# Kernel optimization log

Hardware: AMD Instinct MI355X
Metric: run time of the kernel (lower is better)

Reference implementation:

```python
import jax, jax.numpy as jnp
import numpy as np
import math

HEADS = 8
DIM_HEAD = 64
EMB = 512
GROUPS = 32
EPS = 100000.0  # module's literal default norm_eps


def setup_inputs() -> dict:
    key = jax.random.key(0)
    ks = jax.random.split(key, 11)
    B, D, H, W = 2, EMB, 64, 64
    s = 1.0 / math.sqrt(EMB)
    inp = {
        "input": jax.random.normal(ks[0], (B, D, H, W), dtype=jnp.float32),
        "gn_gamma": jnp.ones((EMB,), dtype=jnp.float32),
        "gn_beta": jnp.zeros((EMB,), dtype=jnp.float32),
        "wq": jax.random.normal(ks[1], (EMB, EMB), dtype=jnp.float32) * s,
        "bq": jax.random.normal(ks[2], (EMB,), dtype=jnp.float32) * 0.01,
        "wk": jax.random.normal(ks[3], (EMB, EMB), dtype=jnp.float32) * s,
        "bk": jax.random.normal(ks[4], (EMB,), dtype=jnp.float32) * 0.01,
        "wv": jax.random.normal(ks[5], (EMB, EMB), dtype=jnp.float32) * s,
        "bv": jax.random.normal(ks[6], (EMB,), dtype=jnp.float32) * 0.01,
        "wo": jax.random.normal(ks[7], (EMB, EMB), dtype=jnp.float32) * s,
        "bo": jax.random.normal(ks[8], (EMB,), dtype=jnp.float32) * 0.01,
    }
    return inp


def reference(input, gn_gamma, gn_beta, wq, bq, wk, bk, wv, bv, wo, bo):
    B, D, H, W = input.shape
    S = H * W
    residual = input

    # GroupNorm(32, D) over (C/G, H, W) per group, affine per-channel
    xg = input.reshape(B, GROUPS, (D // GROUPS) * H * W)
    mu = jnp.mean(xg, axis=-1, keepdims=True)
    var = jnp.var(xg, axis=-1, keepdims=True)
    xn = (xg - mu) / jnp.sqrt(var + EPS)
    xn = xn.reshape(B, D, H, W) * gn_gamma[:, None, None] + gn_beta[:, None, None]

    # (B, D, H, W) -> (B, S, D)
    x = xn.reshape(B, D, S).transpose(0, 2, 1)

    # projections (torch Linear: y = x @ W.T + b)
    q = (x @ wq.T + bq).reshape(B, S, HEADS, DIM_HEAD).transpose(0, 2, 1, 3)
    k = (x @ wk.T + bk).reshape(B, S, HEADS, DIM_HEAD).transpose(0, 2, 1, 3)
    v = (x @ wv.T + bv).reshape(B, S, HEADS, DIM_HEAD).transpose(0, 2, 1, 3)

    scale = 1.0 / math.sqrt(DIM_HEAD)
    scores = jnp.einsum("bhqd,bhkd->bhqk", q * scale, k)  # [B, h, S, S]
    attn = jax.nn.softmax(scores, axis=-1)
    o = jnp.einsum("bhqk,bhkd->bhqd", attn, v)  # [B, h, S, dh]
    o = o.transpose(0, 2, 1, 3).reshape(B, S, D)

    out = o @ wo.T + bo  # [B, S, D]
    out = out.transpose(0, 2, 1).reshape(B, D, H, W)
    return out + residual
```

## Files before the change

### kernel.cpp

```cpp
#include <hip/hip_runtime.h>

#define EMB 512
#define SEQ 4096
#define BATCH 2
#define NH 8
#define DH 64
#define GN_EPS 100000.0f
#define ALPHA 0.125f

typedef __bf16 bf16;
typedef __bf16 bf16x8 __attribute__((ext_vector_type(8)));
typedef float f32x4 __attribute__((ext_vector_type(4)));

typedef __attribute__((address_space(1))) unsigned int u32g;
typedef __attribute__((address_space(3))) unsigned int u32l;
__device__ __forceinline__ void gll16(const void* g, void* l) {
  __builtin_amdgcn_global_load_lds((const u32g*)g, (u32l*)l, 16, 0, 0);
}

__device__ __forceinline__ void stage8(const bf16* g, size_t rowStride, bf16* lds, int lane) {
  const int r = lane >> 3, cc = (lane & 7) ^ r;
  gll16(g + (size_t)r * rowStride + cc * 8, lds + lane * 8);
}
__device__ __forceinline__ bf16x8 frag(const bf16* lds, int r, int cc) {
  return *(const bf16x8*)&lds[(((r << 3) + (cc ^ (r & 7))) << 3)];
}

__global__ __launch_bounds__(256) void stats_k(const float* __restrict__ in,
                                               float* __restrict__ rs,
                                               float* __restrict__ ss) {
  const int row = blockIdx.x;
  const float4* p = (const float4*)(in + (size_t)row * SEQ);
  float s = 0.f, s2 = 0.f;
#pragma unroll
  for (int i = 0; i < 4; ++i) {
    float4 v = p[i * 256 + threadIdx.x];
    s += v.x + v.y + v.z + v.w;
    s2 += v.x * v.x + v.y * v.y + v.z * v.z + v.w * v.w;
  }
#pragma unroll
  for (int o = 32; o > 0; o >>= 1) {
    s += __shfl_down(s, o, 64);
    s2 += __shfl_down(s2, o, 64);
  }
  __shared__ float red[8];
  const int wave = threadIdx.x >> 6, lane = threadIdx.x & 63;
  if (lane == 0) { red[wave] = s; red[4 + wave] = s2; }
  __syncthreads();
  if (threadIdx.x == 0) {
    rs[row] = red[0] + red[1] + red[2] + red[3];
    ss[row] = red[4] + red[5] + red[6] + red[7];
  }
}

__global__ __launch_bounds__(256) void prep_k(const float* __restrict__ wq, const float* __restrict__ wk,
                                              const float* __restrict__ wv, const float* __restrict__ wo,
                                              const float* __restrict__ bv,
                                              const float* __restrict__ rs, const float* __restrict__ ss,
                                              const float* __restrict__ gamma, const float* __restrict__ beta,
                                              bf16* __restrict__ wqt, bf16* __restrict__ wkb,
                                              bf16* __restrict__ wvb, bf16* __restrict__ wob,
                                              float* __restrict__ kxa, float* __restrict__ vsuma) {
  __shared__ float t[64][65];
  __shared__ float xs[1024];
  __shared__ float gmu[64], grs[64];
  const int y = blockIdx.y, tid = threadIdx.x;
  if (y < 8) {
    const int c0 = blockIdx.x * 64, r0 = y * 64;
#pragma unroll
    for (int p = 0; p < 16; ++p) {
      int lin = p * 256 + tid;
      int rl = lin >> 6, cl = lin & 63;
      t[rl][cl] = wq[(size_t)(r0 + rl) * EMB + c0 + cl];
    }
    __syncthreads();
#pragma unroll
    for (int p = 0; p < 16; ++p) {
      int lin = p * 256 + tid;
      int cl = lin >> 6, rl = lin & 63;
      wqt[(size_t)(c0 + cl) * EMB + r0 + rl] = (bf16)t[rl][cl];
    }
  } else {
    const int wi = y - 8;
    const float* W = wi == 0 ? wk : wi == 1 ? wv : wo;
    bf16* WO = wi == 0 ? wkb : wi == 1 ? wvb : wob;
    if (wi < 2) {
      if (tid < 64) {
        float s = 0.f, s2 = 0.f;
#pragma unroll
        for (int c = 0; c < 16; ++c) { s += rs[tid * 16 + c]; s2 += ss[tid * 16 + c]; }
        float mu = s * (1.f / 65536.f);
        float var = s2 * (1.f / 65536.f) - mu * mu;
        gmu[tid] = mu;
        grs[tid] = rsqrtf(var + GN_EPS);
      }
      __syncthreads();
      for (int idx = tid; idx < 1024; idx += 256) {
        int d = idx & 511;
        float s = grs[idx >> 4] * gamma[d];
        float tt = beta[d] - gmu[idx >> 4] * s;
        xs[idx] = s * rs[idx] + 4096.f * tt;
      }
      __syncthreads();
    }
    const int n = blockIdx.x * 64 + (tid >> 2);
    const float* Wr = W + (size_t)n * EMB;
    float dot0 = 0.f, dot1 = 0.f;
    const int dq = (tid & 3) * 128;
    for (int d = dq; d < dq + 128; d += 4) {
      float4 w4 = *(const float4*)&Wr[d];
      if (wi < 2) {
        float4 x0 = *(const float4*)&xs[d];
        float4 x1 = *(const float4*)&xs[EMB + d];
        dot0 += w4.x * x0.x + w4.y * x0.y + w4.z * x0.z + w4.w * x0.w;
        dot1 += w4.x * x1.x + w4.y * x1.y + w4.z * x1.z + w4.w * x1.w;
      }
      bf16 r[4] = {(bf16)w4.x, (bf16)w4.y, (bf16)w4.z, (bf16)w4.w};
      *(uint2*)&WO[(size_t)n * EMB + d] = *(uint2*)r;
    }
    if (wi < 2) {
      dot0 += __shfl_xor(dot0, 1, 4); dot0 += __shfl_xor(dot0, 2, 4);
      dot1 += __shfl_xor(dot1, 1, 4); dot1 += __shfl_xor(dot1, 2, 4);
      if ((tid & 3) == 0) {
        if (wi == 0) { kxa[n] = dot0; kxa[EMB + n] = dot1; }
        else { vsuma[n] = dot0 + 4096.f * bv[n]; vsuma[EMB + n] = dot1 + 4096.f * bv[n]; }
      }
    }
  }
}

__global__ __launch_bounds__(256) void nx_k(const float* __restrict__ in,
                                            const float* __restrict__ rs,
                                            const float* __restrict__ ss,
                                            const float* __restrict__ gamma,
                                            const float* __restrict__ beta,
                                            bf16* __restrict__ xds,
                                            bf16* __restrict__ xsd) {
  __shared__ float t[64][65];
  __shared__ float gmu4[4], grs4[4], scl[64], ttl[64];
  const int s0 = blockIdx.x * 64, d0 = blockIdx.y * 64, b = blockIdx.z;
  const int tid = threadIdx.x;
  if (tid < 4) {
    float s = 0.f, s2 = 0.f;
    int base = b * EMB + d0 + tid * 16;
#pragma unroll
    for (int c = 0; c < 16; ++c) { s += rs[base + c]; s2 += ss[base + c]; }
    float mu = s * (1.f / 65536.f);
    float var = s2 * (1.f / 65536.f) - mu * mu;
    gmu4[tid] = mu;
    grs4[tid] = rsqrtf(var + GN_EPS);
  }
  __syncthreads();
  if (tid < 64) {
    int d = d0 + tid;
    float s = grs4[tid >> 4] * gamma[d];
    scl[tid] = s;
    ttl[tid] = beta[d] - gmu4[tid >> 4] * s;
  }
  __syncthreads();
#pragma unroll
  for (int p = 0; p < 16; ++p) {
    int lin = p * 256 + tid;
    int dl = lin >> 6, sl = lin & 63;
    size_t idx = ((size_t)b * EMB + d0 + dl) * SEQ + s0 + sl;
    float v = in[idx] * scl[dl] + ttl[dl];
    t[dl][sl] = v;
    xds[idx] = (bf16)v;
  }
  __syncthreads();
#pragma unroll
  for (int p = 0; p < 16; ++p) {
    int lin = p * 256 + tid;
    int sl = lin >> 6, dl = lin & 63;
    xsd[((size_t)b * SEQ + s0 + sl) * EMB + d0 + dl] = (bf16)t[dl][sl];
  }
}

__global__ __launch_bounds__(256) void graw2_k(const bf16* __restrict__ xds,
                                               float* __restrict__ pG) {
  __shared__ __align__(16) bf16 As[64 * 64];
  __shared__ __align__(16) bf16 Bs[64 * 64];
  int ti = 0, rem = blockIdx.x;
  while (rem >= 8 - ti) { rem -= 8 - ti; ++ti; }
  const int i0 = ti * 64, j0 = (ti + rem) * 64;
  const int kc = blockIdx.y, b = blockIdx.z;
  const bf16* X = xds + (size_t)b * EMB * SEQ;
  const int tid = threadIdx.x;
  const int wave = tid >> 6, lane = tid & 63, l16 = lane & 15, quad = lane >> 4;
  f32x4 acc[4] = {};
  for (int k0 = kc * 512; k0 < kc * 512 + 512; k0 += 64) {
#pragma unroll
    for (int p = 0; p < 2; ++p) {
      int g = wave * 2 + p;
      stage8(&X[(size_t)(i0 + g * 8) * SEQ + k0], SEQ, &As[g * 512], lane);
      stage8(&X[(size_t)(j0 + g * 8) * SEQ + k0], SEQ, &Bs[g * 512], lane);
    }
    __syncthreads();
#pragma unroll
    for (int kt = 0; kt < 2; ++kt) {
      bf16x8 af = frag(As, wave * 16 + l16, kt * 4 + quad);
#pragma unroll
      for (int nt = 0; nt < 4; ++nt) {
        bf16x8 bb = frag(Bs, nt * 16 + l16, kt * 4 + quad);
        acc[nt] = __builtin_amdgcn_mfma_f32_16x16x32_bf16(af, bb, acc[nt], 0, 0, 0);
      }
    }
    __syncthreads();
  }
  float* pg = pG + ((size_t)(b * 8 + kc) * 36 + blockIdx.x) * 4096;
#pragma unroll
  for (int nt = 0; nt < 4; ++nt)
#pragma unroll
    for (int r = 0; r < 4; ++r)
      pg[(wave * 16 + quad * 4 + r) * 64 + nt * 16 + l16] = acc[nt][r];
}

__global__ __launch_bounds__(256) void gsum_k(const float* __restrict__ pG,
                                              bf16* __restrict__ G) {
  const int b = blockIdx.x >> 10;
  const int e = ((blockIdx.x & 1023) << 8) + threadIdx.x;
  const int i = e >> 9, j = e & 511;
  int ti = i >> 6, tj = j >> 6, row = i & 63, col = j & 63;
  if (ti > tj) { int tmp = ti; ti = tj; tj = tmp; tmp = row; row = col; col = tmp; }
  const int tile = ti * 8 - (ti * (ti - 1)) / 2 + (tj - ti);
  const float* p = pG + (size_t)b * 8 * 36 * 4096 + (size_t)tile * 4096 + row * 64 + col;
  float s = 0.f;
#pragma unroll
  for (int kc = 0; kc < 8; ++kc) s += p[(size_t)kc * 36 * 4096];
  G[(size_t)b * 262144 + e] = (bf16)s;
}

__global__ __launch_bounds__(256) void t2pt_k(const bf16* __restrict__ wkb,
                                              const bf16* __restrict__ G,
                                              const bf16* __restrict__ wvb,
                                              float* __restrict__ pPt) {
  __shared__ __align__(16) bf16 As[64 * 64];
  __shared__ __align__(16) bf16 Bs[64 * 64];
  __shared__ __align__(16) bf16 Ps[4 * 16 * 72];
  const int n0 = blockIdx.x * 64, h = blockIdx.y, b = blockIdx.z;
  const int bh = b * NH + h;
  const int tid = threadIdx.x;
  const int wave = tid >> 6, lane = tid & 63, l16 = lane & 15, quad = lane >> 4;
  bf16* Pw = &Ps[wave * 16 * 72];
  f32x4 acc[4] = {};
  for (int k0 = 0; k0 < EMB; k0 += 64) {
#pragma unroll
    for (int p = 0; p < 2; ++p) {
      int g = wave * 2 + p;
      stage8(&wkb[(size_t)(h * DH + g * 8) * EMB + k0], EMB, &As[g * 512], lane);
      stage8(&G[((size_t)b * EMB + n0 + g * 8) * EMB + k0], EMB, &Bs[g * 512], lane);
    }
    __syncthreads();
#pragma unroll
    for (int kt = 0; kt < 2; ++kt) {
      bf16x8 af = frag(As, wave * 16 + l16, kt * 4 + quad);
#pragma unroll
      for (int nt = 0; nt < 4; ++nt) {
        bf16x8 bb = frag(Bs, nt * 16 + l16, kt * 4 + quad);
        acc[nt] = __builtin_amdgcn_mfma_f32_16x16x32_bf16(af, bb, acc[nt], 0, 0, 0);
      }
    }
    __syncthreads();
  }
#pragma unroll
  for (int nt = 0; nt < 4; ++nt)
#pragma unroll
    for (int r = 0; r < 4; ++r)
      Pw[(quad * 4 + r) * 72 + nt * 16 + l16] = (bf16)acc[nt][r];
#pragma unroll
  for (int p = 0; p < 2; ++p) {
    int g = wave * 2 + p;
    stage8(&wvb[(size_t)(h * DH + g * 8) * EMB + n0], EMB, &Bs[g * 512], lane);
  }
  __syncthreads();
  f32x4 accP[4] = {};
#pragma unroll
  for (int kt = 0; kt < 2; ++kt) {
    bf16x8 pf = *(const bf16x8*)&Pw[l16 * 72 + kt * 32 + quad * 8];
#pragma unroll
    for (int nt = 0; nt < 4; ++nt) {
      bf16x8 bb = frag(Bs, nt * 16 + l16, kt * 4 + quad);
      accP[nt] = __builtin_amdgcn_mfma_f32_16x16x32_bf16(pf, bb, accP[nt], 0, 0, 0);
    }
  }
  float* pp = pPt + ((size_t)bh * 8 + blockIdx.x) * 4096;
#pragma unroll
  for (int nt = 0; nt < 4; ++nt)
#pragma unroll
    for (int r = 0; r < 4; ++r)
      pp[(wave * 16 + quad * 4 + r) * 64 + nt * 16 + l16] = accP[nt][r];
}

__global__ __launch_bounds__(256) void ptsum_k(const float* __restrict__ pPt,
                                               const float* __restrict__ bk,
                                               const float* __restrict__ bv,
                                               const float* __restrict__ kxa,
                                               const float* __restrict__ vsuma,
                                               bf16* __restrict__ Pt) {
  const int bh = blockIdx.x;
  const int b = bh >> 3, h = bh & 7;
  const float sfac = ALPHA / 4096.f;
  for (int e = threadIdx.x; e < 4096; e += 256) {
    int kd = e >> 6, vd = e & 63;
    const float* p = pPt + (size_t)bh * 8 * 4096 + e;
    float s = 0.f;
#pragma unroll
    for (int nt = 0; nt < 8; ++nt) s += p[nt * 4096];
    float bvv = bv[h * DH + vd];
    float bkv = bk[h * DH + kd];
    float vx = vsuma[b * EMB + h * DH + vd] - 4096.f * bvv;
    float val = s + kxa[b * EMB + h * DH + kd] * bvv + bkv * vx + 4096.f * bkv * bvv;
    Pt[(size_t)bh * 4096 + e] = (bf16)(val * sfac);
  }
}

__global__ __launch_bounds__(256) void fchain_k(const bf16* __restrict__ wob,
                                                const bf16* __restrict__ Pt,
                                                const bf16* __restrict__ wqt,
                                                const float* __restrict__ wo,
                                                const float* __restrict__ bo,
                                                const float* __restrict__ bq,
                                                const float* __restrict__ vsuma,
                                                bf16* __restrict__ F,
                                                float* __restrict__ cst) {
  __shared__ __align__(16) bf16 Awo[64 * 64];
  __shared__ __align__(16) bf16 Bp[64 * 64];
  __shared__ __align__(16) bf16 Bwq[64 * 64];
  __shared__ __align__(16) bf16 Ps[4 * 16 * 72];
  __shared__ float yc[512];
  const int i0 = blockIdx.x * 64, j0 = blockIdx.y * 64, b = blockIdx.z;
  const int tid = threadIdx.x;
  const int wave = tid >> 6, lane = tid & 63, l16 = lane & 15, quad = lane >> 4;
  bf16* Pw = &Ps[wave * 16 * 72];
  f32x4 accF[4] = {};
  for (int h = 0; h < NH; ++h) {
    __syncthreads();
#pragma unroll
    for (int p = 0; p < 2; ++p) {
      int g = wave * 2 + p;
      stage8(&wob[(size_t)(i0 + g * 8) * EMB + h * DH], EMB, &Awo[g * 512], lane);
      stage8(&Pt[((size_t)(b * NH + h) * DH + g * 8) * DH], DH, &Bp[g * 512], lane);
      stage8(&wqt[(size_t)(j0 + g * 8) * EMB + h * DH], EMB, &Bwq[g * 512], lane);
    }
    __syncthreads();
    f32x4 at[4] = {};
#pragma unroll
    for (int kt = 0; kt < 2; ++kt) {
      bf16x8 af = frag(Awo, wave * 16 + l16, kt * 4 + quad);
#pragma unroll
      for (int nt = 0; nt < 4; ++nt) {
        bf16x8 bb = frag(Bp, nt * 16 + l16, kt * 4 + quad);
        at[nt] = __builtin_amdgcn_mfma_f32_16x16x32_bf16(af, bb, at[nt], 0, 0, 0);
      }
    }
#pragma unroll
    for (int nt = 0; nt < 4; ++nt)
#pragma unroll
      for (int r = 0; r < 4; ++r)
        Pw[(quad * 4 + r) * 72 + nt * 16 + l16] = (bf16)at[nt][r];
#pragma unroll
    for (int kt = 0; kt < 2; ++kt) {
      bf16x8 pf = *(const bf16x8*)&Pw[l16 * 72 + kt * 32 + quad * 8];
#pragma unroll
      for (int nt = 0; nt < 4; ++nt) {
        bf16x8 bb = frag(Bwq, nt * 16 + l16, kt * 4 + quad);
        accF[nt] = __builtin_amdgcn_mfma_f32_16x16x32_bf16(pf, bb, accF[nt], 0, 0, 0);
      }
    }
  }
#pragma unroll
  for (int nt = 0; nt < 4; ++nt)
#pragma unroll
    for (int r = 0; r < 4; ++r)
      F[((size_t)b * EMB + i0 + wave * 16 + quad * 4 + r) * EMB + j0 + nt * 16 + l16] =
          (bf16)accF[nt][r];
  if (j0 == 0) {
    __syncthreads();
    for (int e = tid; e < 512; e += 256) {
      int h = e >> 6, vd = e & 63;
      const bf16* pp = &Pt[(size_t)(b * NH + h) * DH * DH + vd];
      const float* bqh = &bq[h * DH];
      float a = 0.f;
#pragma unroll 8
      for (int kd = 0; kd < 64; ++kd) a += (float)pp[kd * DH] * bqh[kd];
      yc[e] = vsuma[b * EMB + e] * (1.f / 4096.f) + a;
    }
    __syncthreads();
    const int row = i0 + (tid >> 2);
    const float* wr = &wo[(size_t)row * EMB + (tid & 3) * 128];
    const float* yq = &yc[(tid & 3) * 128];
    float a = 0.f;
    for (int e = 0; e < 128; e += 4) {
      float4 w4 = *(const float4*)&wr[e];
      a += w4.x * yq[e] + w4.y * yq[e + 1] + w4.z * yq[e + 2] + w4.w * yq[e + 3];
    }
    a += __shfl_xor(a, 1, 4);
    a += __shfl_xor(a, 2, 4);
    if ((tid & 3) == 0) cst[b * EMB + row] = bo[row] + a;
  }
}

__global__ __launch_bounds__(256) void final_k(const bf16* __restrict__ F,
                                               const bf16* __restrict__ xsd,
                                               const float* __restrict__ cst,
                                               const float* __restrict__ in,
                                               float* __restrict__ out) {
  __shared__ __align__(16) bf16 As[128 * 64];
  __shared__ __align__(16) bf16 Bs[64 * 64];
  const int m0 = blockIdx.x * 128, s0 = blockIdx.y * 64, b = blockIdx.z;
  const bf16* Fb = F + (size_t)b * EMB * EMB;
  const bf16* Xb = xsd + (size_t)b * SEQ * EMB;
  const int tid = threadIdx.x;
  const int wave = tid >> 6, lane = tid & 63, l16 = lane & 15, quad = lane >> 4;
  f32x4 acc[2][4] = {};
  for (int k0 = 0; k0 < EMB; k0 += 64) {
#pragma unroll
    for (int p = 0; p < 4; ++p) {
      int g = wave * 4 + p;
      stage8(&Fb[(size_t)(m0 + g * 8) * EMB + k0], EMB, &As[g * 512], lane);
    }
#pragma unroll
    for (int p = 0; p < 2; ++p) {
      int g = wave * 2 + p;
      stage8(&Xb[(size_t)(s0 + g * 8) * EMB + k0], EMB, &Bs[g * 512], lane);
    }
    __syncthreads();
#pragma unroll
    for (int kt = 0; kt < 2; ++kt) {
      bf16x8 a0 = frag(As, wave * 32 + l16, kt * 4 + quad);
      bf16x8 a1 = frag(As, wave * 32 + 16 + l16, kt * 4 + quad);
#pragma unroll
      for (int nt = 0; nt < 4; ++nt) {
        bf16x8 bb = frag(Bs, nt * 16 + l16, kt * 4 + quad);
        acc[0][nt] = __builtin_amdgcn_mfma_f32_16x16x32_bf16(a0, bb, acc[0][nt], 0, 0, 0);
        acc[1][nt] = __builtin_amdgcn_mfma_f32_16x16x32_bf16(a1, bb, acc[1][nt], 0, 0, 0);
      }
    }
    __syncthreads();
  }
#pragma unroll
  for (int mt = 0; mt < 2; ++mt) {
    int rowl = m0 + wave * 32 + mt * 16 + quad * 4;
#pragma unroll
    for (int r = 0; r < 4; ++r) {
      float cv = cst[b * EMB + rowl + r];
      size_t base = ((size_t)b * EMB + rowl + r) * SEQ + s0;
#pragma unroll
      for (int nt = 0; nt < 4; ++nt) {
        size_t idx = base + nt * 16 + l16;
        out[idx] = in[idx] + cv + acc[mt][nt][r];
      }
    }
  }
}

extern "C" void kernel_launch(void* const* d_in, const int* in_sizes, int n_in,
                              void* d_out, int out_size, void* d_ws, size_t ws_size,
                              hipStream_t stream) {
  const float* inp = (const float*)d_in[0];
  const float* gam = (const float*)d_in[1];
  const float* bet = (const float*)d_in[2];
  const float* wq = (const float*)d_in[3];
  const float* bq = (const float*)d_in[4];
  const float* wk = (const float*)d_in[5];
  const float* bk = (const float*)d_in[6];
  const float* wv = (const float*)d_in[7];
  const float* bv = (const float*)d_in[8];
  const float* wo = (const float*)d_in[9];
  const float* bo = (const float*)d_in[10];
  float* out = (float*)d_out;
  (void)in_sizes; (void)n_in; (void)out_size; (void)ws_size;

  char* ws = (char*)d_ws;
  size_t off = 0;
  auto take = [&](size_t bytes) -> char* {
    char* p = ws + off;
    off += (bytes + 255) & ~(size_t)255;
    return p;
  };
  float* rs = (float*)take(1024 * 4);
  float* ssq = (float*)take(1024 * 4);
  float* kxa = (float*)take(1024 * 4);
  float* vsuma = (float*)take(1024 * 4);
  float* cst = (float*)take(1024 * 4);
  const size_t WB = (size_t)EMB * EMB * sizeof(bf16);
  bf16* wkb = (bf16*)take(WB);
  bf16* wvb = (bf16*)take(WB);
  bf16* wob = (bf16*)take(WB);
  bf16* wqtb = (bf16*)take(WB);
  const size_t XB = (size_t)BATCH * SEQ * EMB * sizeof(bf16);
  bf16* xds = (bf16*)take(XB);
  bf16* xsd = (bf16*)take(XB);
  float* pG = (float*)take((size_t)BATCH * 8 * 36 * 4096 * sizeof(float));
  bf16* G = (bf16*)take((size_t)BATCH * EMB * EMB * sizeof(bf16));
  float* pPt = (float*)take((size_t)16 * 8 * 4096 * sizeof(float));
  bf16* Pt = (bf16*)take((size_t)16 * 4096 * sizeof(bf16));
  bf16* F = (bf16*)take((size_t)BATCH * EMB * EMB * sizeof(bf16));

  stats_k<<<1024, 256, 0, stream>>>(inp, rs, ssq);
  prep_k<<<dim3(8, 11), 256, 0, stream>>>(wq, wk, wv, wo, bv, rs, ssq, gam, bet,
                                          wqtb, wkb, wvb, wob, kxa, vsuma);
  nx_k<<<dim3(64, 8, 2), 256, 0, stream>>>(inp, rs, ssq, gam, bet, xds, xsd);
  graw2_k<<<dim3(36, 8, 2), 256, 0, stream>>>(xds, pG);
  gsum_k<<<2048, 256, 0, stream>>>(pG, G);
  t2pt_k<<<dim3(8, 8, 2), 256, 0, stream>>>(wkb, G, wvb, pPt);
  ptsum_k<<<16, 256, 0, stream>>>(pPt, bk, bv, kxa, vsuma, Pt);
  fchain_k<<<dim3(8, 8, 2), 256, 0, stream>>>(wob, Pt, wqtb, wo, bo, bq, vsuma, F, cst);
  final_k<<<dim3(4, 64, 2), 256, 0, stream>>>(F, xsd, cst, inp, out);
}
```

Measured before the change: 177.3 us.

## Merge prep and normalize kernels, fold split-K reductions into last-block epilogues

Merges the weight-prep and normalize/transpose kernels into one launch. It also removes the separate gsum and ptsum reduction kernels: the last block to finish each tile, found with an atomic counter zeroed in stats_k, does the split-K sum inside graw2_k and t2pt_k. t2pt_k is split over K into twice as many blocks for more parallelism. This cuts the launch count from nine to six and raises occupancy, at the cost of atomics, thread fences and serialized tail reductions in the final blocks.

```diff
diff --git a/kernel.cpp b/kernel.cpp
--- a/kernel.cpp
+++ b/kernel.cpp
@@ -28,7 +28,9 @@
 
 __global__ __launch_bounds__(256) void stats_k(const float* __restrict__ in,
                                                float* __restrict__ rs,
-                                               float* __restrict__ ss) {
+                                               float* __restrict__ ss,
+                                               int* __restrict__ cnt) {
+  if (blockIdx.x == 0 && threadIdx.x < 88) cnt[threadIdx.x] = 0;
   const int row = blockIdx.x;
   const float4* p = (const float4*)(in + (size_t)row * SEQ);
   float s = 0.f, s2 = 0.f;
@@ -53,133 +55,132 @@
   }
 }
 
-__global__ __launch_bounds__(256) void prep_k(const float* __restrict__ wq, const float* __restrict__ wk,
-                                              const float* __restrict__ wv, const float* __restrict__ wo,
-                                              const float* __restrict__ bv,
-                                              const float* __restrict__ rs, const float* __restrict__ ss,
-                                              const float* __restrict__ gamma, const float* __restrict__ beta,
-                                              bf16* __restrict__ wqt, bf16* __restrict__ wkb,
-                                              bf16* __restrict__ wvb, bf16* __restrict__ wob,
-                                              float* __restrict__ kxa, float* __restrict__ vsuma) {
+__global__ __launch_bounds__(256) void nxprep_k(const float* __restrict__ in,
+                                                const float* __restrict__ rs, const float* __restrict__ ss,
+                                                const float* __restrict__ gamma, const float* __restrict__ beta,
+                                                const float* __restrict__ wq, const float* __restrict__ wk,
+                                                const float* __restrict__ wv, const float* __restrict__ wo,
+                                                const float* __restrict__ bv,
+                                                bf16* __restrict__ xds, bf16* __restrict__ xsd,
+                                                bf16* __restrict__ wqt, bf16* __restrict__ wkb,
+                                                bf16* __restrict__ wvb, bf16* __restrict__ wob,
+                                                float* __restrict__ kxa, float* __restrict__ vsuma) {
   __shared__ float t[64][65];
   __shared__ float xs[1024];
   __shared__ float gmu[64], grs[64];
-  const int y = blockIdx.y, tid = threadIdx.x;
-  if (y < 8) {
-    const int c0 = blockIdx.x * 64, r0 = y * 64;
+  const int id = blockIdx.x, tid = threadIdx.x;
+  if (id < 1024) {
+    const int b = id >> 9, rem = id & 511;
+    const int d0 = (rem >> 6) * 64, s0 = (rem & 63) * 64;
+    if (tid < 4) {
+      float s = 0.f, s2 = 0.f;
+      int base = b * EMB + d0 + tid * 16;
+#pragma unroll
+      for (int c = 0; c < 16; ++c) { s += rs[base + c]; s2 += ss[base + c]; }
+      float mu = s * (1.f / 65536.f);
+      float var = s2 * (1.f / 65536.f) - mu * mu;
+      gmu[tid] = mu;
+      grs[tid] = rsqrtf(var + GN_EPS);
+    }
+    __syncthreads();
+    if (tid < 64) {
+      int d = d0 + tid;
+      float s = grs[tid >> 4] * gamma[d];
+      xs[tid] = s;
+      xs[64 + tid] = beta[d] - gmu[tid >> 4] * s;
+    }
+    __syncthreads();
 #pragma unroll
     for (int p = 0; p < 16; ++p) {
       int lin = p * 256 + tid;
-      int rl = lin >> 6, cl = lin & 63;
-      t[rl][cl] = wq[(size_t)(r0 + rl) * EMB + c0 + cl];
+      int dl = lin >> 6, sl = lin & 63;
+      size_t idx = ((size_t)b * EMB + d0 + dl) * SEQ + s0 + sl;
+      float v = in[idx] * xs[dl] + xs[64 + dl];
+      t[dl][sl] = v;
+      xds[idx] = (bf16)v;
     }
     __syncthreads();
 #pragma unroll
     for (int p = 0; p < 16; ++p) {
       int lin = p * 256 + tid;
-      int cl = lin >> 6, rl = lin & 63;
-      wqt[(size_t)(c0 + cl) * EMB + r0 + rl] = (bf16)t[rl][cl];
+      int sl = lin >> 6, dl = lin & 63;
+      xsd[((size_t)b * SEQ + s0 + sl) * EMB + d0 + dl] = (bf16)t[dl][sl];
     }
   } else {
-    const int wi = y - 8;
-    const float* W = wi == 0 ? wk : wi == 1 ? wv : wo;
-    bf16* WO = wi == 0 ? wkb : wi == 1 ? wvb : wob;
-    if (wi < 2) {
-      if (tid < 64) {
-        float s = 0.f, s2 = 0.f;
-#pragma unroll
-        for (int c = 0; c < 16; ++c) { s += rs[tid * 16 + c]; s2 += ss[tid * 16 + c]; }
-        float mu = s * (1.f / 65536.f);
-        float var = s2 * (1.f / 65536.f) - mu * mu;
-        gmu[tid] = mu;
-        grs[tid] = rsqrtf(var + GN_EPS);
+    const int r = id - 1024;
+    const int bx = r & 7, y = r >> 3;
+    if (y < 8) {
+      const int c0 = bx * 64, r0 = y * 64;
+#pragma unroll
+      for (int p = 0; p < 16; ++p) {
+        int lin = p * 256 + tid;
+        int rl = lin >> 6, cl = lin & 63;
+        t[rl][cl] = wq[(size_t)(r0 + rl) * EMB + c0 + cl];
       }
       __syncthreads();
-      for (int idx = tid; idx < 1024; idx += 256) {
-        int d = idx & 511;
-        float s = grs[idx >> 4] * gamma[d];
-        float tt = beta[d] - gmu[idx >> 4] * s;
-        xs[idx] = s * rs[idx] + 4096.f * tt;
-      }
-      __syncthreads();
-    }
-    const int n = blockIdx.x * 64 + (tid >> 2);
-    const float* Wr = W + (size_t)n * EMB;
-    float dot0 = 0.f, dot1 = 0.f;
-    const int dq = (tid & 3) * 128;
-    for (int d = dq; d < dq + 128; d += 4) {
-      float4 w4 = *(const float4*)&Wr[d];
+#pragma unroll
+      for (int p = 0; p < 16; ++p) {
+        int lin = p * 256 + tid;
+        int cl = lin >> 6, rl = lin & 63;
+        wqt[(size_t)(c0 + cl) * EMB + r0 + rl] = (bf16)t[rl][cl];
+      }
+    } else {
+      const int wi = y - 8;
+      const float* W = wi == 0 ? wk : wi == 1 ? wv : wo;
+      bf16* WO = wi == 0 ? wkb : wi == 1 ? wvb : wob;
       if (wi < 2) {
-        float4 x0 = *(const float4*)&xs[d];
-        float4 x1 = *(const float4*)&xs[EMB + d];
-        dot0 += w4.x * x0.x + w4.y * x0.y + w4.z * x0.z + w4.w * x0.w;
-        dot1 += w4.x * x1.x + w4.y * x1.y + w4.z * x1.z + w4.w * x1.w;
-      }
-      bf16 r[4] = {(bf16)w4.x, (bf16)w4.y, (bf16)w4.z, (bf16)w4.w};
-      *(uint2*)&WO[(size_t)n * EMB + d] = *(uint2*)r;
-    }
-    if (wi < 2) {
-      dot0 += __shfl_xor(dot0, 1, 4); dot0 += __shfl_xor(dot0, 2, 4);
-      dot1 += __shfl_xor(dot1, 1, 4); dot1 += __shfl_xor(dot1, 2, 4);
-      if ((tid & 3) == 0) {
-        if (wi == 0) { kxa[n] = dot0; kxa[EMB + n] = dot1; }
-        else { vsuma[n] = dot0 + 4096.f * bv[n]; vsuma[EMB + n] = dot1 + 4096.f * bv[n]; }
-      }
-    }
-  }
-}
-
-__global__ __launch_bounds__(256) void nx_k(const float* __restrict__ in,
-                                            const float* __restrict__ rs,
-                                            const float* __restrict__ ss,
-                                            const float* __restrict__ gamma,
-                                            const float* __restrict__ beta,
-                                            bf16* __restrict__ xds,
-                                            bf16* __restrict__ xsd) {
-  __shared__ float t[64][65];
-  __shared__ float gmu4[4], grs4[4], scl[64], ttl[64];
-  const int s0 = blockIdx.x * 64, d0 = blockIdx.y * 64, b = blockIdx.z;
-  const int tid = threadIdx.x;
-  if (tid < 4) {
-    float s = 0.f, s2 = 0.f;
-    int base = b * EMB + d0 + tid * 16;
-#pragma unroll
-    for (int c = 0; c < 16; ++c) { s += rs[base + c]; s2 += ss[base + c]; }
-    float mu = s * (1.f / 65536.f);
-    float var = s2 * (1.f / 65536.f) - mu * mu;
-    gmu4[tid] = mu;
-    grs4[tid] = rsqrtf(var + GN_EPS);
-  }
-  __syncthreads();
-  if (tid < 64) {
-    int d = d0 + tid;
-    float s = grs4[tid >> 4] * gamma[d];
-    scl[tid] = s;
-    ttl[tid] = beta[d] - gmu4[tid >> 4] * s;
-  }
-  __syncthreads();
-#pragma unroll
-  for (int p = 0; p < 16; ++p) {
-    int lin = p * 256 + tid;
-    int dl = lin >> 6, sl = lin & 63;
-    size_t idx = ((size_t)b * EMB + d0 + dl) * SEQ + s0 + sl;
-    float v = in[idx] * scl[dl] + ttl[dl];
-    t[dl][sl] = v;
-    xds[idx] = (bf16)v;
-  }
-  __syncthreads();
-#pragma unroll
-  for (int p = 0; p < 16; ++p) {
-    int lin = p * 256 + tid;
-    int sl = lin >> 6, dl = lin & 63;
-    xsd[((size_t)b * SEQ + s0 + sl) * EMB + d0 + dl] = (bf16)t[dl][sl];
+        if (tid < 64) {
+          float s = 0.f, s2 = 0.f;
+#pragma unroll
+          for (int c = 0; c < 16; ++c) { s += rs[tid * 16 + c]; s2 += ss[tid * 16 + c]; }
+          float mu = s * (1.f / 65536.f);
+          float var = s2 * (1.f / 65536.f) - mu * mu;
+          gmu[tid] = mu;
+          grs[tid] = rsqrtf(var + GN_EPS);
+        }
+        __syncthreads();
+        for (int idx = tid; idx < 1024; idx += 256) {
+          int d = idx & 511;
+          float s = grs[idx >> 4] * gamma[d];
+          float tt = beta[d] - gmu[idx >> 4] * s;
+          xs[idx] = s * rs[idx] + 4096.f * tt;
+        }
+        __syncthreads();
+      }
+      const int n = bx * 64 + (tid >> 2);
+      const float* Wr = W + (size_t)n * EMB;
+      float dot0 = 0.f, dot1 = 0.f;
+      const int dq = (tid & 3) * 128;
+      for (int d = dq; d < dq + 128; d += 4) {
+        float4 w4 = *(const float4*)&Wr[d];
+        if (wi < 2) {
+          float4 x0 = *(const float4*)&xs[d];
+          float4 x1 = *(const float4*)&xs[EMB + d];
+          dot0 += w4.x * x0.x + w4.y * x0.y + w4.z * x0.z + w4.w * x0.w;
+          dot1 += w4.x * x1.x + w4.y * x1.y + w4.z * x1.z + w4.w * x1.w;
+        }
+        bf16 rr[4] = {(bf16)w4.x, (bf16)w4.y, (bf16)w4.z, (bf16)w4.w};
+        *(uint2*)&WO[(size_t)n * EMB + d] = *(uint2*)rr;
+      }
+      if (wi < 2) {
+        dot0 += __shfl_xor(dot0, 1, 4); dot0 += __shfl_xor(dot0, 2, 4);
+        dot1 += __shfl_xor(dot1, 1, 4); dot1 += __shfl_xor(dot1, 2, 4);
+        if ((tid & 3) == 0) {
+          if (wi == 0) { kxa[n] = dot0; kxa[EMB + n] = dot1; }
+          else { vsuma[n] = dot0 + 4096.f * bv[n]; vsuma[EMB + n] = dot1 + 4096.f * bv[n]; }
+        }
+      }
+    }
   }
 }
 
 __global__ __launch_bounds__(256) void graw2_k(const bf16* __restrict__ xds,
-                                               float* __restrict__ pG) {
+                                               float* __restrict__ pG,
+                                               bf16* __restrict__ G,
+                                               int* __restrict__ cnt) {
   __shared__ __align__(16) bf16 As[64 * 64];
   __shared__ __align__(16) bf16 Bs[64 * 64];
+  __shared__ int lastFlag;
   int ti = 0, rem = blockIdx.x;
   while (rem >= 8 - ti) { rem -= 8 - ti; ++ti; }
   const int i0 = ti * 64, j0 = (ti + rem) * 64;
@@ -213,37 +214,46 @@
 #pragma unroll
     for (int r = 0; r < 4; ++r)
       pg[(wave * 16 + quad * 4 + r) * 64 + nt * 16 + l16] = acc[nt][r];
-}
-
-__global__ __launch_bounds__(256) void gsum_k(const float* __restrict__ pG,
-                                              bf16* __restrict__ G) {
-  const int b = blockIdx.x >> 10;
-  const int e = ((blockIdx.x & 1023) << 8) + threadIdx.x;
-  const int i = e >> 9, j = e & 511;
-  int ti = i >> 6, tj = j >> 6, row = i & 63, col = j & 63;
-  if (ti > tj) { int tmp = ti; ti = tj; tj = tmp; tmp = row; row = col; col = tmp; }
-  const int tile = ti * 8 - (ti * (ti - 1)) / 2 + (tj - ti);
-  const float* p = pG + (size_t)b * 8 * 36 * 4096 + (size_t)tile * 4096 + row * 64 + col;
-  float s = 0.f;
-#pragma unroll
-  for (int kc = 0; kc < 8; ++kc) s += p[(size_t)kc * 36 * 4096];
-  G[(size_t)b * 262144 + e] = (bf16)s;
+  __threadfence();
+  if (tid == 0) lastFlag = (atomicAdd(&cnt[b * 36 + blockIdx.x], 1) == 7);
+  __syncthreads();
+  if (lastFlag) {
+    __threadfence();
+    for (int e = tid; e < 4096; e += 256) {
+      const float* p = pG + ((size_t)b * 8 * 36 + blockIdx.x) * 4096 + e;
+      float s = 0.f;
+#pragma unroll
+      for (int k = 0; k < 8; ++k) s += p[(size_t)k * 36 * 4096];
+      int row = e >> 6, col = e & 63;
+      bf16 v = (bf16)s;
+      G[((size_t)b * EMB + i0 + row) * EMB + j0 + col] = v;
+      if (i0 != j0) G[((size_t)b * EMB + j0 + col) * EMB + i0 + row] = v;
+    }
+  }
 }
 
 __global__ __launch_bounds__(256) void t2pt_k(const bf16* __restrict__ wkb,
                                               const bf16* __restrict__ G,
                                               const bf16* __restrict__ wvb,
-                                              float* __restrict__ pPt) {
+                                              const float* __restrict__ bk,
+                                              const float* __restrict__ bv,
+                                              const float* __restrict__ kxa,
+                                              const float* __restrict__ vsuma,
+                                              float* __restrict__ pPt,
+                                              bf16* __restrict__ Pt,
+                                              int* __restrict__ cnt) {
   __shared__ __align__(16) bf16 As[64 * 64];
   __shared__ __align__(16) bf16 Bs[64 * 64];
   __shared__ __align__(16) bf16 Ps[4 * 16 * 72];
-  const int n0 = blockIdx.x * 64, h = blockIdx.y, b = blockIdx.z;
+  __shared__ int lastFlag;
+  const int n0 = blockIdx.x * 64, h = blockIdx.y;
+  const int b = blockIdx.z & 1, kc = blockIdx.z >> 1;
   const int bh = b * NH + h;
   const int tid = threadIdx.x;
   const int wave = tid >> 6, lane = tid & 63, l16 = lane & 15, quad = lane >> 4;
   bf16* Pw = &Ps[wave * 16 * 72];
   f32x4 acc[4] = {};
-  for (int k0 = 0; k0 < EMB; k0 += 64) {
+  for (int k0 = kc * 256; k0 < kc * 256 + 256; k0 += 64) {
 #pragma unroll
     for (int p = 0; p < 2; ++p) {
       int g = wave * 2 + p;
@@ -283,34 +293,30 @@
       accP[nt] = __builtin_amdgcn_mfma_f32_16x16x32_bf16(pf, bb, accP[nt], 0, 0, 0);
     }
   }
-  float* pp = pPt + ((size_t)bh * 8 + blockIdx.x) * 4096;
+  float* pp = pPt + ((size_t)bh * 16 + blockIdx.x * 2 + kc) * 4096;
 #pragma unroll
   for (int nt = 0; nt < 4; ++nt)
 #pragma unroll
     for (int r = 0; r < 4; ++r)
       pp[(wave * 16 + quad * 4 + r) * 64 + nt * 16 + l16] = accP[nt][r];
-}
-
-__global__ __launch_bounds__(256) void ptsum_k(const float* __restrict__ pPt,
-                                               const float* __restrict__ bk,
-                                               const float* __restrict__ bv,
-                                               const float* __restrict__ kxa,
-                                               const float* __restrict__ vsuma,
-                                               bf16* __restrict__ Pt) {
-  const int bh = blockIdx.x;
-  const int b = bh >> 3, h = bh & 7;
-  const float sfac = ALPHA / 4096.f;
-  for (int e = threadIdx.x; e < 4096; e += 256) {
-    int kd = e >> 6, vd = e & 63;
-    const float* p = pPt + (size_t)bh * 8 * 4096 + e;
-    float s = 0.f;
-#pragma unroll
-    for (int nt = 0; nt < 8; ++nt) s += p[nt * 4096];
-    float bvv = bv[h * DH + vd];
-    float bkv = bk[h * DH + kd];
-    float vx = vsuma[b * EMB + h * DH + vd] - 4096.f * bvv;
-    float val = s + kxa[b * EMB + h * DH + kd] * bvv + bkv * vx + 4096.f * bkv * bvv;
-    Pt[(size_t)bh * 4096 + e] = (bf16)(val * sfac);
+  __threadfence();
+  if (tid == 0) lastFlag = (atomicAdd(&cnt[72 + bh], 1) == 15);
+  __syncthreads();
+  if (lastFlag) {
+    __threadfence();
+    const float sfac = ALPHA / 4096.f;
+    for (int e = tid; e < 4096; e += 256) {
+      int kd = e >> 6, vd = e & 63;
+      const float* p = pPt + (size_t)bh * 16 * 4096 + e;
+      float s = 0.f;
+#pragma unroll
+      for (int nt = 0; nt < 16; ++nt) s += p[nt * 4096];
+      float bvv = bv[h * DH + vd];
+      float bkv = bk[h * DH + kd];
+      float vx = vsuma[b * EMB + h * DH + vd] - 4096.f * bvv;
+      float val = s + kxa[b * EMB + h * DH + kd] * bvv + bkv * vx + 4096.f * bkv * bvv;
+      Pt[(size_t)bh * 4096 + e] = (bf16)(val * sfac);
+    }
   }
 }
 
@@ -483,6 +489,7 @@
   float* kxa = (float*)take(1024 * 4);
   float* vsuma = (float*)take(1024 * 4);
   float* cst = (float*)take(1024 * 4);
+  int* cnt = (int*)take(88 * 4);
   const size_t WB = (size_t)EMB * EMB * sizeof(bf16);
   bf16* wkb = (bf16*)take(WB);
   bf16* wvb = (bf16*)take(WB);
@@ -493,18 +500,15 @@
   bf16* xsd = (bf16*)take(XB);
   float* pG = (float*)take((size_t)BATCH * 8 * 36 * 4096 * sizeof(float));
   bf16* G = (bf16*)take((size_t)BATCH * EMB * EMB * sizeof(bf16));
-  float* pPt = (float*)take((size_t)16 * 8 * 4096 * sizeof(float));
+  float* pPt = (float*)take((size_t)16 * 16 * 4096 * sizeof(float));
   bf16* Pt = (bf16*)take((size_t)16 * 4096 * sizeof(bf16));
   bf16* F = (bf16*)take((size_t)BATCH * EMB * EMB * sizeof(bf16));
 
-  stats_k<<<1024, 256, 0, stream>>>(inp, rs, ssq);
-  prep_k<<<dim3(8, 11), 256, 0, stream>>>(wq, wk, wv, wo, bv, rs, ssq, gam, bet,
-                                          wqtb, wkb, wvb, wob, kxa, vsuma);
-  nx_k<<<dim3(64, 8, 2), 256, 0, stream>>>(inp, rs, ssq, gam, bet, xds, xsd);
-  graw2_k<<<dim3(36, 8, 2), 256, 0, stream>>>(xds, pG);
-  gsum_k<<<2048, 256, 0, stream>>>(pG, G);
-  t2pt_k<<<dim3(8, 8, 2), 256, 0, stream>>>(wkb, G, wvb, pPt);
-  ptsum_k<<<16, 256, 0, stream>>>(pPt, bk, bv, kxa, vsuma, Pt);
+  stats_k<<<1024, 256, 0, stream>>>(inp, rs, ssq, cnt);
+  nxprep_k<<<1112, 256, 0, stream>>>(inp, rs, ssq, gam, bet, wq, wk, wv, wo, bv,
+                                     xds, xsd, wqtb, wkb, wvb, wob, kxa, vsuma);
+  graw2_k<<<dim3(36, 8, 2), 256, 0, stream>>>(xds, pG, G, cnt);
+  t2pt_k<<<dim3(8, 8, 4), 256, 0, stream>>>(wkb, G, wvb, bk, bv, kxa, vsuma, pPt, Pt, cnt);
   fchain_k<<<dim3(8, 8, 2), 256, 0, stream>>>(wob, Pt, wqtb, wo, bo, bq, vsuma, F, cst);
   final_k<<<dim3(4, 64, 2), 256, 0, stream>>>(F, xsd, cst, inp, out);
 }
```

Measured after the change: 269.0 us. +51.7%, slower.
